# Optimization experiments

Hardware: AMD Instinct MI355X
Metric: run time of the kernel (lower is better)

The kernel has to match this reference:

```python
import jax, jax.numpy as jnp
import numpy as np

B, S, E = 2, 2048, 2048
N_HEAD = 16
HEAD_DIM = E // N_HEAD  # 128
MP_NUM = 4              # hardcoded in the torch forward
ROTARY_DIM = 64


def setup_inputs() -> dict:
    key = jax.random.key(0)
    k1, k2, k3 = jax.random.split(key, 3)
    return {
        "hidden_states": jax.random.normal(k1, (B, S, E), jnp.float32) * 0.02,
        "w_qkv": jax.random.normal(k2, (3 * E, E), jnp.float32) * 0.02,  # torch Linear weight [out,in]
        "w_out": jax.random.normal(k3, (E, E), jnp.float32) * 0.02,
    }


def _rotate_every_two(x):
    # (..., d) -> interleaved (-x2, x1) as in GPT-J/CodeGen
    x1 = x[..., 0::2]
    x2 = x[..., 1::2]
    return jnp.stack((-x2, x1), axis=-1).reshape(x.shape)


def reference(hidden_states, w_qkv, w_out):
    b, s, e = hidden_states.shape
    local = e // MP_NUM  # per-mp-shard channel count

    # qkv projection (no bias), then mp_num split: order is (query, value, key)
    qkv = jnp.einsum("bse,fe->bsf", hidden_states, w_qkv)  # [B,S,3E]
    qkv = qkv.reshape(b, s, MP_NUM, 3 * local)
    q = qkv[..., :local].reshape(b, s, N_HEAD, HEAD_DIM)
    v = qkv[..., local:2 * local].reshape(b, s, N_HEAD, HEAD_DIM)
    k = qkv[..., 2 * local:].reshape(b, s, N_HEAD, HEAD_DIM)

    # partial rotary (rotate-every-two) on first ROTARY_DIM channels
    inv_freq = 1.0 / (10000.0 ** (jnp.arange(0, ROTARY_DIM, 2, dtype=jnp.float32) / ROTARY_DIM))
    freqs = jnp.arange(s, dtype=jnp.float32)[:, None] * inv_freq[None, :]  # [S, R/2]
    sin = jnp.repeat(jnp.sin(freqs), 2, axis=-1)[None, :, None, :]  # [1,S,1,R]
    cos = jnp.repeat(jnp.cos(freqs), 2, axis=-1)[None, :, None, :]

    def rope(x):
        x_rot = x[..., :ROTARY_DIM]
        x_pass = x[..., ROTARY_DIM:]
        x_rot = x_rot * cos + _rotate_every_two(x_rot) * sin
        return jnp.concatenate([x_rot, x_pass], axis=-1)

    q = rope(q)
    k = rope(k)

    # [B,S,H,D] -> [B,H,S,D]
    q = q.transpose(0, 2, 1, 3)
    k = k.transpose(0, 2, 1, 3)
    v = v.transpose(0, 2, 1, 3)

    scale = jnp.sqrt(jnp.asarray(HEAD_DIM, dtype=q.dtype))
    scores = jnp.einsum("bhqd,bhkd->bhqk", q, k) / scale  # [B,H,S,S]
    causal = jnp.tril(jnp.ones((s, s), dtype=bool))
    scores = jnp.where(causal[None, None, :, :], scores, jnp.finfo(scores.dtype).min)
    attn = jax.nn.softmax(scores, axis=-1)

    out = jnp.einsum("bhqk,bhkd->bhqd", attn, v)  # [B,H,S,D]
    out = out.transpose(0, 2, 1, 3).reshape(b, s, e)  # merge heads
    return jnp.einsum("bse,fe->bsf", out, w_out)  # out_proj (no bias)
```

## Files before the change

### kernel.cpp

```cpp
#include <hip/hip_runtime.h>

typedef unsigned short u16;
typedef unsigned int u32;
typedef __attribute__((ext_vector_type(4))) float f32x4;
typedef __attribute__((ext_vector_type(8))) short s16x8;
typedef __attribute__((ext_vector_type(4))) unsigned int u32x4;

#define DEVI static __device__ __forceinline__


#define ROPE_C (-13.287712379549449f / 32.0f)
#define QSCALE 0.12751743f

DEVI u16 f2bf(float f) {
  u32 u = __float_as_uint(f);
  return (u16)((u + 0x7FFFu + ((u >> 16) & 1u)) >> 16);
}
DEVI float bf2f(u16 h) { return __uint_as_float(((u32)h) << 16); }

DEVI void async_copy16(const u16* g, u16* l) {
  __builtin_amdgcn_global_load_lds((__attribute__((address_space(1))) void*)g,
                                   (__attribute__((address_space(3))) void*)l, 16, 0, 0);
}

__global__ __launch_bounds__(256) void cast3_kernel(
    const float* __restrict__ s0, u16* __restrict__ d0, int n0,
    const float* __restrict__ s1, u16* __restrict__ d1, int n1,
    const float* __restrict__ s2, u16* __restrict__ d2, int n2) {
  int i = blockIdx.x * 256 + threadIdx.x;
  const float* s;
  u16* d;
  if (i < n0) {
    s = s0; d = d0;
  } else if (i < n0 + n1) {
    s = s1; d = d1; i -= n0;
  } else if (i < n0 + n1 + n2) {
    s = s2; d = d2; i -= n0 + n1;
  } else {
    return;
  }
  const float4 v = ((const float4*)s)[i];
  ushort4 o;
  o.x = f2bf(v.x); o.y = f2bf(v.y); o.z = f2bf(v.z); o.w = f2bf(v.w);
  ((ushort4*)d)[i] = o;
}

template <int EPI>
__global__ __launch_bounds__(256, 3) void gemm_bt_kernel(
    const u16* __restrict__ A, const u16* __restrict__ Bm, int K, int N,
    float* __restrict__ C, u16* __restrict__ qo, u16* __restrict__ ko, u16* __restrict__ vo) {
  __shared__ __attribute__((aligned(16))) u16 As[3][128 * 32];
  __shared__ __attribute__((aligned(16))) u16 Bs[3][128 * 32];
  const int tid = threadIdx.x;
  const int w = tid >> 6, lane = tid & 63;
  const int quad = lane >> 4, l16 = lane & 15;
  const int wrow = (w >> 1) * 64, wcol = (w & 1) * 64;
  const long tileM = (long)blockIdx.y * 128;
  const long tileN = (long)blockIdx.x * 128;

  f32x4 acc[4][4];
#pragma unroll
  for (int i = 0; i < 4; ++i)
#pragma unroll
    for (int j = 0; j < 4; ++j) acc[i][j] = f32x4{0.f, 0.f, 0.f, 0.f};

  const u16* aptr[2];
  const u16* bptr[2];
  int ldso[2];
#pragma unroll
  for (int c = 0; c < 2; ++c) {
    const int r0 = (w * 2 + c) * 16;
    const int row = r0 + (lane >> 2);
    const int colsw = (((lane & 3) ^ ((row >> 1) & 3)) << 3);
    aptr[c] = A + (tileM + row) * (long)K + colsw;
    bptr[c] = Bm + (tileN + row) * (long)K + colsw;
    ldso[c] = r0 * 32;
  }

  auto stage = [&](int k0, int buf) {
#pragma unroll
    for (int c = 0; c < 2; ++c) {
      async_copy16(aptr[c] + k0, &As[buf][ldso[c]]);
      async_copy16(bptr[c] + k0, &Bs[buf][ldso[c]]);
    }
  };

  stage(0, 0);
  stage(32, 1);

  const int psw = (quad ^ ((l16 >> 1) & 3)) << 3;

  int bt = 0;
  for (int k0 = 0; k0 < K; k0 += 32) {
    if (k0 + 32 < K)
      __builtin_amdgcn_s_waitcnt(0x0f74);
    else
      __builtin_amdgcn_s_waitcnt(0x0f70);
    __builtin_amdgcn_s_barrier();
    if (k0 + 64 < K) stage(k0 + 64, bt == 0 ? 2 : bt - 1);

    s16x8 af[4], bfr[4];
#pragma unroll
    for (int i = 0; i < 4; ++i)
      af[i] = *(const s16x8*)(&As[bt][(wrow + i * 16 + l16) * 32 + psw]);
#pragma unroll
    for (int j = 0; j < 4; ++j)
      bfr[j] = *(const s16x8*)(&Bs[bt][(wcol + j * 16 + l16) * 32 + psw]);
#pragma unroll
    for (int i = 0; i < 4; ++i)
#pragma unroll
      for (int j = 0; j < 4; ++j)
        acc[i][j] = __builtin_amdgcn_mfma_f32_16x16x32_bf16(af[i], bfr[j], acc[i][j], 0, 0, 0);
    bt = bt == 2 ? 0 : bt + 1;
  }

  const int b = (int)(tileM >> 11);
#pragma unroll
  for (int i = 0; i < 4; ++i) {
#pragma unroll
    for (int j = 0; j < 4; ++j) {
      const int rowb = (int)((tileM + wrow + i * 16 + quad * 4) & 2047);
      if (EPI == 0) {
#pragma unroll
        for (int r = 0; r < 4; ++r) {
          const long row = tileM + wrow + i * 16 + quad * 4 + r;
          C[row * N + tileN + wcol + j * 16 + l16] = acc[i][j][r];
        }
      } else {
        const long col0 = tileN + wcol + j * 16;
        const int mp = (int)(col0 / 1536);
        const int cc0 = (int)(col0 - (long)mp * 1536);
        const int part = cc0 >> 9;
        const int idx0 = cc0 & 511;
        const int head = mp * 4 + (idx0 >> 7);
        const int dim0 = idx0 & 127;
        const int dim = dim0 + l16;
        const long bh = (long)(b * 16 + head);
        if (part == 1) {
#pragma unroll
          for (int r = 0; r < 4; ++r)
            vo[(bh * 128 + dim) * 2048 + rowb + r] = f2bf(acc[i][j][r]);
        } else {
          float y[4];
          if (part == 2 && dim0 < 64) {
            const int jj = dim >> 1;
            const float inv = exp2f((float)jj * ROPE_C);
#pragma unroll
            for (int r = 0; r < 4; ++r) {
              const float v = acc[i][j][r];
              const float pv = __shfl_xor(v, 1, 64);
              const float ang = (float)(rowb + r) * inv;
              const float sn = __sinf(ang), cs = __cosf(ang);
              y[r] = (l16 & 1) ? (v * cs + pv * sn) : (v * cs - pv * sn);
            }
          } else {
#pragma unroll
            for (int r = 0; r < 4; ++r) y[r] = acc[i][j][r];
          }
          u16* dst = (part == 0) ? qo : ko;
#pragma unroll
          for (int r = 0; r < 4; ++r)
            dst[(bh * 2048 + rowb + r) * 128 + dim] = f2bf(y[r]);
        }
      }
    }
  }
}

__global__ __launch_bounds__(512, 2) void gemm_qkv256_kernel(
    const u16* __restrict__ A, const u16* __restrict__ Bm, int K,
    u16* __restrict__ qo, u16* __restrict__ ko, u16* __restrict__ vo) {
  __shared__ __attribute__((aligned(16))) u16 As[2][2][128 * 64];
  __shared__ __attribute__((aligned(16))) u16 Bs[2][2][128 * 64];
  const int tid = threadIdx.x;
  const int w = tid >> 6, lane = tid & 63;
  const int quad = lane >> 4, l16 = lane & 15;
  const int wm = w >> 2, wn = w & 3;
  const long tileM = (long)blockIdx.y * 256;
  const long tileN = (long)blockIdx.x * 256;

  f32x4 acc[8][4];
#pragma unroll
  for (int i = 0; i < 8; ++i)
#pragma unroll
    for (int j = 0; j < 4; ++j) acc[i][j] = f32x4{0.f, 0.f, 0.f, 0.f};

  const int rowoff = lane >> 3;
  const int swz = ((lane & 7) ^ rowoff) << 3;
  const u16* aBase = A + (tileM + w * 16 + rowoff) * (long)K + swz;
  const u16* bBase = Bm + (tileN + w * 16 + rowoff) * (long)K + swz;
  const int ldsb = (w * 16) * 64;

  auto stageA2 = [&](int t) {
    const int buf = t & 1;
    const long k0 = (long)t << 6;
#pragma unroll
    for (int h = 0; h < 2; ++h)
#pragma unroll
      for (int c = 0; c < 2; ++c)
        async_copy16(aBase + (long)(h * 128 + c * 8) * K + k0,
                     &As[buf][h][ldsb + c * 8 * 64]);
  };
  auto stageB2 = [&](int t) {
    const int buf = t & 1;
    const long k0 = (long)t << 6;
#pragma unroll
    for (int h = 0; h < 2; ++h)
#pragma unroll
      for (int c = 0; c < 2; ++c)
        async_copy16(bBase + (long)(h * 128 + c * 8) * K + k0,
                     &Bs[buf][h][ldsb + c * 8 * 64]);
  };

  const int gsw = l16 & 7;
  auto rdA = [&](int buf, int i, int kk) -> s16x8 {
    return *(const s16x8*)(
        &As[buf][wm][(i * 16 + l16) * 64 + ((((kk << 2) + quad) ^ gsw) << 3)]);
  };
  auto rdB = [&](int buf, int j, int kk) -> s16x8 {
    return *(const s16x8*)(
        &Bs[buf][wn >> 1][(((wn & 1) * 64) + j * 16 + l16) * 64 +
                          ((((kk << 2) + quad) ^ gsw) << 3)]);
  };

  const int NT = K >> 6;
  stageB2(0); stageA2(0);
  stageB2(1); stageA2(1);
  __builtin_amdgcn_s_waitcnt(0x0f78);
  __builtin_amdgcn_s_barrier();

  for (int t = 0; t < NT; ++t) {
    const int buf = t & 1;
    const bool pf = (t + 2 < NT);
    s16x8 a[4][2], b0[2][2], b1[2][2];

#pragma unroll
    for (int i = 0; i < 4; ++i)
#pragma unroll
      for (int kk = 0; kk < 2; ++kk) a[i][kk] = rdA(buf, i, kk);
#pragma unroll
    for (int j = 0; j < 2; ++j)
#pragma unroll
      for (int kk = 0; kk < 2; ++kk) b0[j][kk] = rdB(buf, j, kk);
    __builtin_amdgcn_s_barrier();
    __builtin_amdgcn_s_setprio(1);
#pragma unroll
    for (int i = 0; i < 4; ++i)
#pragma unroll
      for (int j = 0; j < 2; ++j)
#pragma unroll
        for (int kk = 0; kk < 2; ++kk)
          acc[i][j] =
              __builtin_amdgcn_mfma_f32_16x16x32_bf16(a[i][kk], b0[j][kk], acc[i][j], 0, 0, 0);
    __builtin_amdgcn_s_setprio(0);
    __builtin_amdgcn_s_barrier();

#pragma unroll
    for (int j = 0; j < 2; ++j)
#pragma unroll
      for (int kk = 0; kk < 2; ++kk) b1[j][kk] = rdB(buf, 2 + j, kk);
    __builtin_amdgcn_s_barrier();
    __builtin_amdgcn_s_setprio(1);
#pragma unroll
    for (int i = 0; i < 4; ++i)
#pragma unroll
      for (int j = 0; j < 2; ++j)
#pragma unroll
        for (int kk = 0; kk < 2; ++kk)
          acc[i][2 + j] = __builtin_amdgcn_mfma_f32_16x16x32_bf16(a[i][kk], b1[j][kk],
                                                                  acc[i][2 + j], 0, 0, 0);
    __builtin_amdgcn_s_setprio(0);
    __builtin_amdgcn_s_barrier();

    if (pf) stageB2(t + 2);
#pragma unroll
    for (int i = 0; i < 4; ++i)
#pragma unroll
      for (int kk = 0; kk < 2; ++kk) a[i][kk] = rdA(buf, 4 + i, kk);
    __builtin_amdgcn_s_barrier();
    __builtin_amdgcn_s_setprio(1);
#pragma unroll
    for (int i = 0; i < 4; ++i)
#pragma unroll
      for (int j = 0; j < 2; ++j)
#pragma unroll
        for (int kk = 0; kk < 2; ++kk)
          acc[4 + i][j] = __builtin_amdgcn_mfma_f32_16x16x32_bf16(a[i][kk], b0[j][kk],
                                                                  acc[4 + i][j], 0, 0, 0);
    __builtin_amdgcn_s_setprio(0);
    __builtin_amdgcn_s_barrier();

    if (pf) stageA2(t + 2);
    __builtin_amdgcn_s_barrier();
    __builtin_amdgcn_s_setprio(1);
#pragma unroll
    for (int i = 0; i < 4; ++i)
#pragma unroll
      for (int j = 0; j < 2; ++j)
#pragma unroll
        for (int kk = 0; kk < 2; ++kk)
          acc[4 + i][2 + j] = __builtin_amdgcn_mfma_f32_16x16x32_bf16(
              a[i][kk], b1[j][kk], acc[4 + i][2 + j], 0, 0, 0);
    __builtin_amdgcn_s_setprio(0);
    if (pf)
      __builtin_amdgcn_s_waitcnt(0x0f78);
    else
      __builtin_amdgcn_s_waitcnt(0x0f70);
    __builtin_amdgcn_s_barrier();
  }

  const int b = (int)(tileM >> 11);
#pragma unroll
  for (int i = 0; i < 8; ++i) {
#pragma unroll
    for (int j = 0; j < 4; ++j) {
      const int rowb = (int)((tileM + wm * 128 + i * 16 + quad * 4) & 2047);
      const long col0 = tileN + wn * 64 + j * 16;
      const int mp = (int)(col0 / 1536);
      const int cc0 = (int)(col0 - (long)mp * 1536);
      const int part = cc0 >> 9;
      const int idx0 = cc0 & 511;
      const int head = mp * 4 + (idx0 >> 7);
      const int dim0 = idx0 & 127;
      const int dim = dim0 + l16;
      const long bh = (long)(b * 16 + head);
      if (part == 1) {
#pragma unroll
        for (int r = 0; r < 4; ++r)
          vo[(bh * 128 + dim) * 2048 + rowb + r] = f2bf(acc[i][j][r]);
      } else {
        float y[4];
        if (part == 2 && dim0 < 64) {
          const int jj = dim >> 1;
          const float inv = exp2f((float)jj * ROPE_C);
#pragma unroll
          for (int r = 0; r < 4; ++r) {
            const float v = acc[i][j][r];
            const float pv = __shfl_xor(v, 1, 64);
            const float ang = (float)(rowb + r) * inv;
            const float sn = __sinf(ang), cs = __cosf(ang);
            y[r] = (l16 & 1) ? (v * cs + pv * sn) : (v * cs - pv * sn);
          }
        } else {
#pragma unroll
          for (int r = 0; r < 4; ++r) y[r] = acc[i][j][r];
        }
        u16* dst = (part == 0) ? qo : ko;
#pragma unroll
        for (int r = 0; r < 4; ++r)
          dst[(bh * 2048 + rowb + r) * 128 + dim] = f2bf(y[r]);
      }
    }
  }
}

__global__ __launch_bounds__(256, 4) void attn_kernel(
    const u16* __restrict__ q, const u16* __restrict__ k,
    const u16* __restrict__ vT, u16* __restrict__ out) {
  __shared__ __attribute__((aligned(16))) u16 Ks[2][32 * 128];
  __shared__ __attribute__((aligned(16))) u16 Vs[2][128 * 32];
  const int tid = threadIdx.x;
  const int w = tid >> 6, lane = tid & 63;
  const int quad = lane >> 4, l16 = lane & 15;
  const int qt = 31 - (blockIdx.x >> 5);
  const int bh = blockIdx.x & 31;
  const int qbase = qt * 64 + w * 16;

  const u16* qp = q + ((long)bh * 2048 + qbase) * 128;
  const u16* kp = k + (long)bh * 2048 * 128;
  const u16* vp = vT + (long)bh * 128 * 2048;

  const float spos = (float)(qbase + l16);
  s16x8 qf[4];
#pragma unroll
  for (int c = 0; c < 4; ++c) {
    const s16x8 raw = *(const s16x8*)(qp + l16 * 128 + c * 32 + quad * 8);
    s16x8 ov;
    if (c < 2) {
#pragma unroll
      for (int m = 0; m < 4; ++m) {
        const int jj = c * 16 + quad * 4 + m;
        const float inv = exp2f((float)jj * ROPE_C);
        const float ang = spos * inv;
        const float sn = __sinf(ang), cs = __cosf(ang);
        const float x0 = bf2f((u16)raw[2 * m]), x1 = bf2f((u16)raw[2 * m + 1]);
        ov[2 * m] = (short)f2bf((x0 * cs - x1 * sn) * QSCALE);
        ov[2 * m + 1] = (short)f2bf((x1 * cs + x0 * sn) * QSCALE);
      }
    } else {
#pragma unroll
      for (int e = 0; e < 8; ++e) ov[e] = (short)f2bf(bf2f((u16)raw[e]) * QSCALE);
    }
    qf[c] = ov;
  }

  f32x4 acc[8];
#pragma unroll
  for (int d = 0; d < 8; ++d) acc[d] = f32x4{0.f, 0.f, 0.f, 0.f};
  float mrun = -1e30f, lrun = 0.f;

  auto stage = [&](int k0, int buf) {
    const int ko = lane >> 4, cl = lane & 15;
#pragma unroll
    for (int i = 0; i < 2; ++i) {
      const int keyt = w * 8 + i * 4;
      const int key = keyt + ko;
      async_copy16(kp + (long)(k0 + key) * 128 + ((cl ^ (key & 15)) << 3),
                   &Ks[buf][keyt * 128]);
    }
    const int ld = lane >> 2, c4 = lane & 3;
#pragma unroll
    for (int i = 0; i < 2; ++i) {
      const int db = w * 32 + i * 16;
      const int d = db + ld;
      async_copy16(vp + (long)d * 2048 + k0 + ((c4 ^ ((d >> 1) & 3)) << 3),
                   &Vs[buf][db * 32]);
    }
  };

  stage(0, 0);

  const int nt = 2 * qt + 2;
  for (int t = 0; t < nt; ++t) {
    const int k0 = t * 32;
    const u16* Ksc = Ks[t & 1];
    const u16* Vsc = Vs[t & 1];
    __builtin_amdgcn_s_waitcnt(0x0f70);
    __syncthreads();
    if (t + 1 < nt) stage(k0 + 32, (t + 1) & 1);

    f32x4 sc[2];
#pragma unroll
    for (int g = 0; g < 2; ++g) {
      sc[g] = f32x4{0.f, 0.f, 0.f, 0.f};
#pragma unroll
      for (int c = 0; c < 4; ++c) {
        const s16x8 kf = *(const s16x8*)(
            &Ksc[(g * 16 + l16) * 128 + ((((c << 2) + quad) ^ l16) << 3)]);
        sc[g] = __builtin_amdgcn_mfma_f32_16x16x32_bf16(kf, qf[c], sc[g], 0, 0, 0);
      }
    }
    if (k0 + 31 > qbase) {
      const int qrow = qbase + l16;
#pragma unroll
      for (int g = 0; g < 2; ++g) {
        const int keyb = k0 + g * 16 + quad * 4;
#pragma unroll
        for (int r = 0; r < 4; ++r)
          if (keyb + r > qrow) sc[g][r] = -1e30f;
      }
    }
    float mx = fmaxf(fmaxf(fmaxf(sc[0][0], sc[0][1]), fmaxf(sc[0][2], sc[0][3])),
                     fmaxf(fmaxf(sc[1][0], sc[1][1]), fmaxf(sc[1][2], sc[1][3])));
    mx = fmaxf(mx, __shfl_xor(mx, 16, 64));
    mx = fmaxf(mx, __shfl_xor(mx, 32, 64));
    const float mnew = fmaxf(mrun, mx);
    const float alpha = exp2f(mrun - mnew);
    mrun = mnew;
    float p[2][4];
    float sm = 0.f;
#pragma unroll
    for (int g = 0; g < 2; ++g)
#pragma unroll
      for (int r = 0; r < 4; ++r) { p[g][r] = exp2f(sc[g][r] - mnew); sm += p[g][r]; }
    sm += __shfl_xor(sm, 16, 64);
    sm += __shfl_xor(sm, 32, 64);
    lrun = lrun * alpha + sm;
#pragma unroll
    for (int d = 0; d < 8; ++d)
#pragma unroll
      for (int r = 0; r < 4; ++r) acc[d][r] *= alpha;

    u32 pk[2][2];
#pragma unroll
    for (int g = 0; g < 2; ++g) {
      pk[g][0] = (u32)f2bf(p[g][0]) | ((u32)f2bf(p[g][1]) << 16);
      pk[g][1] = (u32)f2bf(p[g][2]) | ((u32)f2bf(p[g][3]) << 16);
    }
    const int la = ((quad & 1) << 5) + l16;
    const int lb = la + 16;
    const u32 a0 = (u32)__shfl((int)pk[0][0], la, 64);
    const u32 a1 = (u32)__shfl((int)pk[0][1], la, 64);
    const u32 a2 = (u32)__shfl((int)pk[0][0], lb, 64);
    const u32 a3 = (u32)__shfl((int)pk[0][1], lb, 64);
    const u32 b0 = (u32)__shfl((int)pk[1][0], la, 64);
    const u32 b1 = (u32)__shfl((int)pk[1][1], la, 64);
    const u32 b2 = (u32)__shfl((int)pk[1][0], lb, 64);
    const u32 b3 = (u32)__shfl((int)pk[1][1], lb, 64);
    const bool hi = quad >= 2;
    const u32x4 pw = {hi ? b0 : a0, hi ? b1 : a1, hi ? b2 : a2, hi ? b3 : a3};
    const s16x8 pf = __builtin_bit_cast(s16x8, pw);

#pragma unroll
    for (int dd = 0; dd < 8; ++dd) {
      const s16x8 vf = *(const s16x8*)(
          &Vsc[(dd * 16 + l16) * 32 + ((quad ^ ((l16 >> 1) & 3)) << 3)]);
      acc[dd] = __builtin_amdgcn_mfma_f32_16x16x32_bf16(vf, pf, acc[dd], 0, 0, 0);
    }
  }

  const int b = bh >> 4, h = bh & 15;
  u16* op = out + ((long)b * 2048 + qbase + l16) * 2048 + h * 128;
  const float inv_l = 1.0f / lrun;
#pragma unroll
  for (int dd = 0; dd < 8; ++dd) {
    ushort4 o4;
    o4.x = f2bf(acc[dd][0] * inv_l);
    o4.y = f2bf(acc[dd][1] * inv_l);
    o4.z = f2bf(acc[dd][2] * inv_l);
    o4.w = f2bf(acc[dd][3] * inv_l);
    *(ushort4*)(op + dd * 16 + quad * 4) = o4;
  }
}

extern "C" void kernel_launch(void* const* d_in, const int* in_sizes, int n_in,
                              void* d_out, int out_size, void* d_ws, size_t ws_size,
                              hipStream_t stream) {
  const float* hidden = (const float*)d_in[0];
  const float* w_qkv = (const float*)d_in[1];
  const float* w_out = (const float*)d_in[2];
  float* out = (float*)d_out;
  char* ws = (char*)d_ws;

  u16* hid_b  = (u16*)(ws + (size_t)0);
  u16* wqkv_b = (u16*)(ws + (size_t)16777216);
  u16* wout_b = (u16*)(ws + (size_t)41943040);
  u16* qb     = (u16*)(ws + (size_t)50331648);
  u16* kb     = (u16*)(ws + (size_t)67108864);
  u16* vb     = (u16*)(ws + (size_t)83886080);
  u16* ao     = (u16*)(ws + (size_t)100663296);

  cast3_kernel<<<24576, 256, 0, stream>>>(hidden, hid_b, 2097152,
                                          w_qkv, wqkv_b, 3145728,
                                          w_out, wout_b, 1048576);

  gemm_qkv256_kernel<<<dim3(24, 16), 512, 0, stream>>>(hid_b, wqkv_b, 2048,
                                                       qb, kb, vb);
  attn_kernel<<<1024, 256, 0, stream>>>(qb, kb, vb, ao);
  gemm_bt_kernel<0><<<dim3(16, 32), 256, 0, stream>>>(ao, wout_b, 2048, 2048,
                                                      out, nullptr, nullptr, nullptr);
}
```

Baseline: 401.8 us.

## Remap QKV GEMM blocks per XCD, reorder MFMAs, add lazy softmax rescale

The QKV GEMM launch becomes a 1D grid whose block ids are remapped so that consecutive tiles land on the same XCD, which is meant to improve L2 reuse. Its MFMA loops are reordered to put kk outermost, and the A-fragment LDS reads are hoisted ahead of the B prefetch. The attention kernel replaces __syncthreads with a raw barrier, interleaves the two QK MFMA chains, adds setprio around the MFMA blocks, and only rescales the accumulator when the row max grows by more than a threshold. The lazy rescale removes most of the per-tile multiplies, but it lets exponents exceed 1 by up to 2^8, which could slightly affect precision in the bf16 P values.

```diff
diff --git a/kernel.cpp b/kernel.cpp
--- a/kernel.cpp
+++ b/kernel.cpp
@@ -176,8 +176,11 @@
   const int w = tid >> 6, lane = tid & 63;
   const int quad = lane >> 4, l16 = lane & 15;
   const int wm = w >> 2, wn = w & 3;
-  const long tileM = (long)blockIdx.y * 256;
-  const long tileN = (long)blockIdx.x * 256;
+
+  const int bid = blockIdx.x;
+  const int id = (bid & 7) * 48 + (bid >> 3);
+  const long tileM = (long)(id & 15) * 256;
+  const long tileN = (long)(id >> 4) * 256;
 
   f32x4 acc[8][4];
 #pragma unroll
@@ -245,11 +248,11 @@
     __builtin_amdgcn_s_barrier();
     __builtin_amdgcn_s_setprio(1);
 #pragma unroll
-    for (int i = 0; i < 4; ++i)
-#pragma unroll
-      for (int j = 0; j < 2; ++j)
-#pragma unroll
-        for (int kk = 0; kk < 2; ++kk)
+    for (int kk = 0; kk < 2; ++kk)
+#pragma unroll
+      for (int i = 0; i < 4; ++i)
+#pragma unroll
+        for (int j = 0; j < 2; ++j)
           acc[i][j] =
               __builtin_amdgcn_mfma_f32_16x16x32_bf16(a[i][kk], b0[j][kk], acc[i][j], 0, 0, 0);
     __builtin_amdgcn_s_setprio(0);
@@ -262,29 +265,29 @@
     __builtin_amdgcn_s_barrier();
     __builtin_amdgcn_s_setprio(1);
 #pragma unroll
-    for (int i = 0; i < 4; ++i)
-#pragma unroll
-      for (int j = 0; j < 2; ++j)
-#pragma unroll
-        for (int kk = 0; kk < 2; ++kk)
+    for (int kk = 0; kk < 2; ++kk)
+#pragma unroll
+      for (int i = 0; i < 4; ++i)
+#pragma unroll
+        for (int j = 0; j < 2; ++j)
           acc[i][2 + j] = __builtin_amdgcn_mfma_f32_16x16x32_bf16(a[i][kk], b1[j][kk],
                                                                   acc[i][2 + j], 0, 0, 0);
     __builtin_amdgcn_s_setprio(0);
     __builtin_amdgcn_s_barrier();
 
+#pragma unroll
+    for (int i = 0; i < 4; ++i)
+#pragma unroll
+      for (int kk = 0; kk < 2; ++kk) a[i][kk] = rdA(buf, 4 + i, kk);
     if (pf) stageB2(t + 2);
-#pragma unroll
-    for (int i = 0; i < 4; ++i)
-#pragma unroll
-      for (int kk = 0; kk < 2; ++kk) a[i][kk] = rdA(buf, 4 + i, kk);
     __builtin_amdgcn_s_barrier();
     __builtin_amdgcn_s_setprio(1);
 #pragma unroll
-    for (int i = 0; i < 4; ++i)
-#pragma unroll
-      for (int j = 0; j < 2; ++j)
-#pragma unroll
-        for (int kk = 0; kk < 2; ++kk)
+    for (int kk = 0; kk < 2; ++kk)
+#pragma unroll
+      for (int i = 0; i < 4; ++i)
+#pragma unroll
+        for (int j = 0; j < 2; ++j)
           acc[4 + i][j] = __builtin_amdgcn_mfma_f32_16x16x32_bf16(a[i][kk], b0[j][kk],
                                                                   acc[4 + i][j], 0, 0, 0);
     __builtin_amdgcn_s_setprio(0);
@@ -294,11 +297,11 @@
     __builtin_amdgcn_s_barrier();
     __builtin_amdgcn_s_setprio(1);
 #pragma unroll
-    for (int i = 0; i < 4; ++i)
-#pragma unroll
-      for (int j = 0; j < 2; ++j)
-#pragma unroll
-        for (int kk = 0; kk < 2; ++kk)
+    for (int kk = 0; kk < 2; ++kk)
+#pragma unroll
+      for (int i = 0; i < 4; ++i)
+#pragma unroll
+        for (int j = 0; j < 2; ++j)
           acc[4 + i][2 + j] = __builtin_amdgcn_mfma_f32_16x16x32_bf16(
               a[i][kk], b1[j][kk], acc[4 + i][2 + j], 0, 0, 0);
     __builtin_amdgcn_s_setprio(0);
@@ -426,20 +429,23 @@
     const u16* Ksc = Ks[t & 1];
     const u16* Vsc = Vs[t & 1];
     __builtin_amdgcn_s_waitcnt(0x0f70);
-    __syncthreads();
+    __builtin_amdgcn_s_barrier();
     if (t + 1 < nt) stage(k0 + 32, (t + 1) & 1);
 
     f32x4 sc[2];
-#pragma unroll
-    for (int g = 0; g < 2; ++g) {
-      sc[g] = f32x4{0.f, 0.f, 0.f, 0.f};
-#pragma unroll
-      for (int c = 0; c < 4; ++c) {
-        const s16x8 kf = *(const s16x8*)(
-            &Ksc[(g * 16 + l16) * 128 + ((((c << 2) + quad) ^ l16) << 3)]);
-        sc[g] = __builtin_amdgcn_mfma_f32_16x16x32_bf16(kf, qf[c], sc[g], 0, 0, 0);
-      }
-    }
+    sc[0] = f32x4{0.f, 0.f, 0.f, 0.f};
+    sc[1] = f32x4{0.f, 0.f, 0.f, 0.f};
+    __builtin_amdgcn_s_setprio(1);
+#pragma unroll
+    for (int c = 0; c < 4; ++c) {
+      const s16x8 kf0 = *(const s16x8*)(
+          &Ksc[(0 * 16 + l16) * 128 + ((((c << 2) + quad) ^ l16) << 3)]);
+      const s16x8 kf1 = *(const s16x8*)(
+          &Ksc[(1 * 16 + l16) * 128 + ((((c << 2) + quad) ^ l16) << 3)]);
+      sc[0] = __builtin_amdgcn_mfma_f32_16x16x32_bf16(kf0, qf[c], sc[0], 0, 0, 0);
+      sc[1] = __builtin_amdgcn_mfma_f32_16x16x32_bf16(kf1, qf[c], sc[1], 0, 0, 0);
+    }
+    __builtin_amdgcn_s_setprio(0);
     if (k0 + 31 > qbase) {
       const int qrow = qbase + l16;
 #pragma unroll
@@ -454,22 +460,25 @@
                      fmaxf(fmaxf(sc[1][0], sc[1][1]), fmaxf(sc[1][2], sc[1][3])));
     mx = fmaxf(mx, __shfl_xor(mx, 16, 64));
     mx = fmaxf(mx, __shfl_xor(mx, 32, 64));
-    const float mnew = fmaxf(mrun, mx);
-    const float alpha = exp2f(mrun - mnew);
-    mrun = mnew;
+    if (__any(mx > mrun + 8.f)) {
+      const float mnew = fmaxf(mrun, mx);
+      const float alpha = exp2f(mrun - mnew);
+      mrun = mnew;
+      lrun *= alpha;
+#pragma unroll
+      for (int d = 0; d < 8; ++d)
+#pragma unroll
+        for (int r = 0; r < 4; ++r) acc[d][r] *= alpha;
+    }
     float p[2][4];
     float sm = 0.f;
 #pragma unroll
     for (int g = 0; g < 2; ++g)
 #pragma unroll
-      for (int r = 0; r < 4; ++r) { p[g][r] = exp2f(sc[g][r] - mnew); sm += p[g][r]; }
+      for (int r = 0; r < 4; ++r) { p[g][r] = exp2f(sc[g][r] - mrun); sm += p[g][r]; }
     sm += __shfl_xor(sm, 16, 64);
     sm += __shfl_xor(sm, 32, 64);
-    lrun = lrun * alpha + sm;
-#pragma unroll
-    for (int d = 0; d < 8; ++d)
-#pragma unroll
-      for (int r = 0; r < 4; ++r) acc[d][r] *= alpha;
+    lrun += sm;
 
     u32 pk[2][2];
 #pragma unroll
@@ -491,12 +500,14 @@
     const u32x4 pw = {hi ? b0 : a0, hi ? b1 : a1, hi ? b2 : a2, hi ? b3 : a3};
     const s16x8 pf = __builtin_bit_cast(s16x8, pw);
 
+    __builtin_amdgcn_s_setprio(1);
 #pragma unroll
     for (int dd = 0; dd < 8; ++dd) {
       const s16x8 vf = *(const s16x8*)(
           &Vsc[(dd * 16 + l16) * 32 + ((quad ^ ((l16 >> 1) & 3)) << 3)]);
       acc[dd] = __builtin_amdgcn_mfma_f32_16x16x32_bf16(vf, pf, acc[dd], 0, 0, 0);
     }
+    __builtin_amdgcn_s_setprio(0);
   }
 
   const int b = bh >> 4, h = bh & 15;
@@ -534,8 +545,7 @@
                                           w_qkv, wqkv_b, 3145728,
                                           w_out, wout_b, 1048576);
 
-  gemm_qkv256_kernel<<<dim3(24, 16), 512, 0, stream>>>(hid_b, wqkv_b, 2048,
-                                                       qb, kb, vb);
+  gemm_qkv256_kernel<<<384, 512, 0, stream>>>(hid_b, wqkv_b, 2048, qb, kb, vb);
   attn_kernel<<<1024, 256, 0, stream>>>(qb, kb, vb, ao);
   gemm_bt_kernel<0><<<dim3(16, 32), 256, 0, stream>>>(ao, wout_b, 2048, 2048,
                                                       out, nullptr, nullptr, nullptr);
```

Result: no change. 395.4 us (-1.6%).
